# Optimization experiments

Measured on AMD Instinct MI355X. Metric: run time of the kernel, lower is better.

## Reference

```python
import jax, jax.numpy as jnp
import numpy as np
from jax import lax


def _conv(x, w, padding):
    # NCHW input, OIHW weights, stride 1, no bias
    return lax.conv_general_dilated(x, w, (1, 1), padding,
                                    dimension_numbers=('NCHW', 'OIHW', 'NCHW'))


def setup_inputs() -> dict:
    key = jax.random.key(0)
    ks = jax.random.split(key, 6)
    B, C, H, W = 16, 512, 40, 40
    return {
        'exemplar': jax.random.normal(ks[0], (B, C, H, W), jnp.float32),
        'query':    jax.random.normal(ks[1], (B, C, H, W), jnp.float32),
        'w_e':  jax.random.normal(ks[2], (256, C, 1, 1), jnp.float32) * 0.01,
        'w_q':  jax.random.normal(ks[3], (256, C, 1, 1), jnp.float32) * 0.01,
        'w_c1': jax.random.normal(ks[4], (C, C, 3, 3), jnp.float32) * 0.01,
        'w_c2': jax.random.normal(ks[5], (C, C, 3, 3), jnp.float32) * 0.01,
    }


def reference(exemplar, query, w_e, w_q, w_c1, w_c2):
    B, C, H, W = query.shape
    N = H * W
    # 1x1 projections to 256-dim correlation space
    q_corr = _conv(query, w_q, 'VALID').reshape(B, -1, N)     # [B,256,N]
    e_corr = _conv(exemplar, w_e, 'VALID').reshape(B, -1, N)  # [B,256,N]
    # A[b, n_exemplar, m_query] = <e_corr[:, n], q_corr[:, m]>
    A = jnp.einsum('bcn,bcm->bnm', e_corr, q_corr)            # [B,N,N]
    # A1 = softmax over exemplar axis, then transpose (torch: softmax(A,dim=1).T)
    A1 = jnp.swapaxes(jax.nn.softmax(A, axis=1), 1, 2)        # [B,N,N]
    # Bm = softmax(A^T, dim=1).T  == softmax(A, axis=2)
    Bm = jnp.swapaxes(jax.nn.softmax(jnp.swapaxes(A, 1, 2), axis=1), 1, 2)
    e_flat = exemplar.reshape(B, C, N)
    q_flat = query.reshape(B, C, N)
    query_att = jnp.matmul(e_flat, A1)   # [B,C,N]
    exemplar_att = jnp.matmul(q_flat, Bm)  # [B,C,N]
    input1_att = _conv(exemplar_att.reshape(B, C, H, W), w_c1, 'SAME')
    input2_att = _conv(query_att.reshape(B, C, H, W), w_c2, 'SAME')
    return jnp.concatenate([input1_att, input2_att], axis=1)  # [B,2C,H,W]
```

## Files before the change

### kernel.cpp

```cpp
#include <hip/hip_runtime.h>

typedef unsigned short u16;
typedef __attribute__((ext_vector_type(8))) short bf16x8;
typedef __attribute__((ext_vector_type(4))) float f32x4;

__device__ __forceinline__ u16 f2bf(float f) {
  union { float f; unsigned u; } v; v.f = f;
  unsigned u = v.u;
  u += 0x7fffu + ((u >> 16) & 1u);
  return (u16)(u >> 16);
}

__device__ __forceinline__ void gll16(const void* g, void* l) {
  __builtin_amdgcn_global_load_lds(
      (const __attribute__((address_space(1))) void*)g,
      (__attribute__((address_space(3))) void*)l, 16, 0, 0);
}

__global__ __launch_bounds__(256) void transp_cast_x2(const float* __restrict__ ex,
                                                      const float* __restrict__ qu,
                                                      u16* __restrict__ xte,
                                                      u16* __restrict__ xtq) {
  __shared__ float t[32][33];
  int z = blockIdx.z;
  int b = z & 15;
  const float* xb = (z < 16 ? ex : qu) + (size_t)b * 819200;
  u16* xtb = (z < 16 ? xte : xtq) + (size_t)b * 819200;
  int n0 = blockIdx.x * 32, c0 = blockIdx.y * 32;
  int tx = threadIdx.x & 31, ty = threadIdx.x >> 5;
#pragma unroll
  for (int k = 0; k < 4; k++) {
    int c = ty + k * 8;
    t[c][tx] = xb[(size_t)(c0 + c) * 1600 + n0 + tx];
  }
  __syncthreads();
#pragma unroll
  for (int k = 0; k < 4; k++) {
    int n = ty + k * 8;
    xtb[(size_t)(n0 + n) * 512 + c0 + tx] = f2bf(t[tx][n]);
  }
}

__global__ void cast_w(const float* __restrict__ we, const float* __restrict__ wq,
                       u16* __restrict__ oe, u16* __restrict__ oq) {
  int i = blockIdx.x * 256 + threadIdx.x;
  oe[i] = f2bf(we[i]);
  oq[i] = f2bf(wq[i]);
}

__global__ void repack_wc(const float* __restrict__ w1, const float* __restrict__ w2,
                          u16* __restrict__ o1, u16* __restrict__ o2) {
  const float* w = blockIdx.y ? w2 : w1;
  u16* wr = blockIdx.y ? o2 : o1;
  int idx = blockIdx.x * 256 + threadIdx.x;
  int o = idx / 4608;
  int r = idx - o * 4608;
  int t = r >> 9;
  int c = r & 511;
  wr[idx] = f2bf(w[o * 4608 + c * 9 + t]);
}

__global__ void zero_mem(uint4* __restrict__ p, long n) {
  long i = (long)blockIdx.x * blockDim.x + threadIdx.x;
  long stride = (long)gridDim.x * blockDim.x;
  uint4 z; z.x = 0; z.y = 0; z.z = 0; z.w = 0;
  for (; i < n; i += stride) p[i] = z;
}

template <int MODE>
__global__ __launch_bounds__(256) void gemm_bt64(
    const u16* __restrict__ A, const u16* __restrict__ B, u16* __restrict__ C,
    const u16* __restrict__ A2, const u16* __restrict__ B2, u16* __restrict__ C2,
    int M, int N, int K, long sA, long sB, long sC) {
  __shared__ u16 lds_a[128 * 64];
  __shared__ u16 lds_b[128 * 64];
  int tid = threadIdx.x;
  int z = blockIdx.z, b = z & 15;
  const u16* Ab = (z < 16 ? A : A2) + (size_t)b * sA;
  const u16* Bb = (z < 16 ? B : B2) + (size_t)b * sB;
  u16* Cb = (z < 16 ? C : C2) + (size_t)b * sC;
  int m0 = blockIdx.x * 128, n0 = blockIdx.y * 128;

  int rsub = tid >> 3;
  int gch = (tid & 7) ^ (rsub & 7);
  long Kb = (long)K * 2;
  const char* pa[4];
  const char* pb[4];
#pragma unroll
  for (int c = 0; c < 4; c++) {
    int ra = m0 + 32 * c + rsub; ra = ra < M ? ra : M - 1;
    int rb = n0 + 32 * c + rsub; rb = rb < N ? rb : N - 1;
    pa[c] = (const char*)Ab + (long)ra * Kb + gch * 16;
    pb[c] = (const char*)Bb + (long)rb * Kb + gch * 16;
  }

  const f32x4 fzero = {0.f, 0.f, 0.f, 0.f};
  f32x4 acc[4][4];
#pragma unroll
  for (int mi = 0; mi < 4; mi++)
#pragma unroll
    for (int ni = 0; ni < 4; ni++) acc[mi][ni] = fzero;

  int wid = tid >> 6, lane = tid & 63;
  int wm = wid & 1, wn = wid >> 1;
  int lrow = lane & 15, lquad = lane >> 4;
  int sl = lrow & 7;

  int ksteps = K >> 6;
  for (int ks = 0; ks < ksteps; ks++) {
#pragma unroll
    for (int c = 0; c < 4; c++) {
      gll16(pa[c], (char*)lds_a + c * 4096 + tid * 16);
      gll16(pb[c], (char*)lds_b + c * 4096 + tid * 16);
      pa[c] += 128; pb[c] += 128;
    }
    __syncthreads();
#pragma unroll
    for (int k2 = 0; k2 < 2; k2++) {
      int sel = ((k2 << 2) | lquad) ^ sl;
      bf16x8 bv[4];
#pragma unroll
      for (int ni = 0; ni < 4; ni++) {
        int rowb = wn * 64 + ni * 16 + lrow;
        bv[ni] = *(const bf16x8*)((const char*)lds_b + rowb * 128 + sel * 16);
      }
#pragma unroll
      for (int mi = 0; mi < 4; mi++) {
        int rowa = wm * 64 + mi * 16 + lrow;
        bf16x8 av = *(const bf16x8*)((const char*)lds_a + rowa * 128 + sel * 16);
#pragma unroll
        for (int ni = 0; ni < 4; ni++)
          acc[mi][ni] =
              __builtin_amdgcn_mfma_f32_16x16x32_bf16(av, bv[ni], acc[mi][ni], 0, 0, 0);
      }
    }
    __syncthreads();
  }

#pragma unroll
  for (int mi = 0; mi < 4; mi++) {
#pragma unroll
    for (int r = 0; r < 4; r++) {
      int i = m0 + wm * 64 + mi * 16 + lquad * 4 + r;
      if (i >= M) continue;
#pragma unroll
      for (int ni = 0; ni < 4; ni++) {
        int j = n0 + wn * 64 + ni * 16 + lrow;
        if (j >= N) continue;
        float v = acc[mi][ni][r];
        if (MODE == 2) {
          int y = i / 40, x = i - y * 40;
          Cb[(size_t)((y + 1) * 42 + (x + 1)) * 512 + j] = f2bf(v);
        } else {
          Cb[(size_t)i * N + j] = f2bf(v);
        }
      }
    }
  }
}

__global__ __launch_bounds__(256) void gemm_corr_exp(
    const u16* __restrict__ A, const u16* __restrict__ B, u16* __restrict__ E,
    u16* __restrict__ ET, float* __restrict__ Zrow, float* __restrict__ Zcol) {
  __shared__ u16 lds_a[128 * 64];
  __shared__ u16 lds_b[128 * 64];
  int tid = threadIdx.x;
  int b = blockIdx.z;
  const u16* Ab = A + (size_t)b * 409600;
  const u16* Bb = B + (size_t)b * 409600;
  u16* Eb = E + (size_t)b * 2560000;
  u16* ETb = ET + (size_t)b * 2560000;
  int m0 = blockIdx.x * 128, n0 = blockIdx.y * 128;

  int rsub = tid >> 3;
  int gch = (tid & 7) ^ (rsub & 7);
  const char* pa[4];
  const char* pb[4];
#pragma unroll
  for (int c = 0; c < 4; c++) {
    int ra = m0 + 32 * c + rsub; ra = ra < 1600 ? ra : 1599;
    int rb = n0 + 32 * c + rsub; rb = rb < 1600 ? rb : 1599;
    pa[c] = (const char*)(Ab + (size_t)ra * 256) + gch * 16;
    pb[c] = (const char*)(Bb + (size_t)rb * 256) + gch * 16;
  }

  const f32x4 fzero = {0.f, 0.f, 0.f, 0.f};
  f32x4 acc[4][4];
#pragma unroll
  for (int mi = 0; mi < 4; mi++)
#pragma unroll
    for (int ni = 0; ni < 4; ni++) acc[mi][ni] = fzero;

  int wid = tid >> 6, lane = tid & 63;
  int wm = wid & 1, wn = wid >> 1;
  int lrow = lane & 15, lquad = lane >> 4;
  int sl = lrow & 7;

  for (int ks = 0; ks < 4; ks++) {
#pragma unroll
    for (int c = 0; c < 4; c++) {
      gll16(pa[c], (char*)lds_a + c * 4096 + tid * 16);
      gll16(pb[c], (char*)lds_b + c * 4096 + tid * 16);
      pa[c] += 128; pb[c] += 128;
    }
    __syncthreads();
#pragma unroll
    for (int k2 = 0; k2 < 2; k2++) {
      int sel = ((k2 << 2) | lquad) ^ sl;
      bf16x8 bv[4];
#pragma unroll
      for (int ni = 0; ni < 4; ni++) {
        int rowb = wn * 64 + ni * 16 + lrow;
        bv[ni] = *(const bf16x8*)((const char*)lds_b + rowb * 128 + sel * 16);
      }
#pragma unroll
      for (int mi = 0; mi < 4; mi++) {
        int rowa = wm * 64 + mi * 16 + lrow;
        bf16x8 av = *(const bf16x8*)((const char*)lds_a + rowa * 128 + sel * 16);
#pragma unroll
        for (int ni = 0; ni < 4; ni++)
          acc[mi][ni] =
              __builtin_amdgcn_mfma_f32_16x16x32_bf16(av, bv[ni], acc[mi][ni], 0, 0, 0);
      }
    }
    __syncthreads();
  }

  const int TS = 136;
  u16* T = lds_a;
  float colacc[4] = {0.f, 0.f, 0.f, 0.f};
#pragma unroll
  for (int s = 0; s < 4; s++) {
    if (wm == (s >> 1)) {
      int smi0 = (s & 1) * 2;
#pragma unroll
      for (int mi2 = 0; mi2 < 2; mi2++) {
        int mi = smi0 + mi2;
        float rowp[4] = {0.f, 0.f, 0.f, 0.f};
#pragma unroll
        for (int ni = 0; ni < 4; ni++) {
          int j = n0 + wn * 64 + ni * 16 + lrow;
          bool jv = j < 1600;
#pragma unroll
          for (int r = 0; r < 4; r++) {
            int i = m0 + wm * 64 + mi * 16 + lquad * 4 + r;
            float e = __expf(acc[mi][ni][r]);
            T[(mi2 * 16 + lquad * 4 + r) * TS + wn * 64 + ni * 16 + lrow] = f2bf(e);
            rowp[r] += jv ? e : 0.f;
            colacc[ni] += (i < 1600) ? e : 0.f;
          }
        }
#pragma unroll
        for (int r = 0; r < 4; r++) {
          float v = rowp[r];
          v += __shfl_xor(v, 1);
          v += __shfl_xor(v, 2);
          v += __shfl_xor(v, 4);
          v += __shfl_xor(v, 8);
          int i = m0 + wm * 64 + mi * 16 + lquad * 4 + r;
          if (lrow == 0 && i < 1600) atomicAdd(&Zrow[b * 1600 + i], v);
        }
      }
    }
    __syncthreads();
#pragma unroll
    for (int p = 0; p < 2; p++) {
      int jj = tid + p * 256;
      int ml = jj >> 4, n8 = jj & 15;
      int gi = m0 + s * 32 + ml, gj = n0 + n8 * 8;
      if (gi < 1600 && gj < 1600)
        *(uint4*)(Eb + (size_t)gi * 1600 + gj) = *(const uint4*)&T[ml * TS + n8 * 8];
    }
#pragma unroll
    for (int p = 0; p < 4; p++) {
      int jj = tid + p * 256;
      int n = jj >> 3, m4 = jj & 7;
      int gm = m0 + s * 32 + m4 * 4, gn = n0 + n;
      if (gn < 1600 && gm < 1600) {
        ushort4 v;
        v.x = T[(m4 * 4 + 0) * TS + n];
        v.y = T[(m4 * 4 + 1) * TS + n];
        v.z = T[(m4 * 4 + 2) * TS + n];
        v.w = T[(m4 * 4 + 3) * TS + n];
        *(ushort4*)(ETb + (size_t)gn * 1600 + gm) = v;
      }
    }
    __syncthreads();
  }
#pragma unroll
  for (int ni = 0; ni < 4; ni++) {
    float v = colacc[ni];
    v += __shfl_xor(v, 16);
    v += __shfl_xor(v, 32);
    int j = n0 + wn * 64 + ni * 16 + lrow;
    if (lquad == 0 && j < 1600) atomicAdd(&Zcol[b * 1600 + j], v);
  }
}

__global__ void scale_div(const float* __restrict__ ex, const float* __restrict__ qu,
                          const float* __restrict__ Zcol, const float* __restrict__ Zrow,
                          u16* __restrict__ ebf, u16* __restrict__ qbf) {
  const float* x; const float* Z; u16* o;
  if (blockIdx.y == 0) { x = ex; Z = Zcol; o = ebf; }
  else { x = qu; Z = Zrow; o = qbf; }
  size_t idx = (size_t)blockIdx.x * 256 + threadIdx.x;
  int b = (int)(idx / 819200);
  int i = (int)(idx % 1600);
  o[idx] = f2bf(x[idx] / Z[b * 1600 + i]);
}

__global__ __launch_bounds__(256) void conv_gemm64(
    const u16* __restrict__ W1, const u16* __restrict__ ATT1,
    const u16* __restrict__ W2, const u16* __restrict__ ATT2,
    float* __restrict__ out) {
  __shared__ u16 lds_a[128 * 64];
  __shared__ u16 lds_b[128 * 64];
  int tid = threadIdx.x;
  int z = blockIdx.z, b = z & 15, sel2 = z >> 4;
  const u16* W = sel2 ? W2 : W1;
  const u16* attb = (sel2 ? ATT2 : ATT1) + (size_t)b * 903168;
  float* outb = out + (size_t)b * 1638400 + (size_t)(sel2 ? 512 : 0) * 1600;
  int p0 = blockIdx.x * 128, o0 = blockIdx.y * 128;

  int rsub = tid >> 3;
  int gch = (tid & 7) ^ (rsub & 7);
  const char* pa[4];
  const char* pb[4];
#pragma unroll
  for (int c = 0; c < 4; c++) {
    int ro = o0 + 32 * c + rsub;
    pa[c] = (const char*)(W + (size_t)ro * 4608) + gch * 16;
    int p = p0 + 32 * c + rsub; p = p < 1600 ? p : 1599;
    int y = p / 40, x = p - y * 40;
    pb[c] = (const char*)(attb + (size_t)(y * 42 + x) * 512) + gch * 16;
  }

  const f32x4 fzero = {0.f, 0.f, 0.f, 0.f};
  f32x4 acc[4][4];
#pragma unroll
  for (int mi = 0; mi < 4; mi++)
#pragma unroll
    for (int ni = 0; ni < 4; ni++) acc[mi][ni] = fzero;

  int wid = tid >> 6, lane = tid & 63;
  int wm = wid & 1, wn = wid >> 1;
  int lrow = lane & 15, lquad = lane >> 4;
  int sl = lrow & 7;

  int tapbyte = 0, dxc = 0;
  for (int t = 0; t < 9; t++) {
#pragma unroll 2
    for (int kc = 0; kc < 8; kc++) {
#pragma unroll
      for (int c = 0; c < 4; c++) {
        gll16(pa[c], (char*)lds_a + c * 4096 + tid * 16);
        gll16(pb[c] + tapbyte + kc * 128, (char*)lds_b + c * 4096 + tid * 16);
        pa[c] += 128;
      }
      __syncthreads();
#pragma unroll
      for (int k2 = 0; k2 < 2; k2++) {
        int sel = ((k2 << 2) | lquad) ^ sl;
        bf16x8 bv[4];
#pragma unroll
        for (int ni = 0; ni < 4; ni++) {
          int rowb = wn * 64 + ni * 16 + lrow;
          bv[ni] = *(const bf16x8*)((const char*)lds_b + rowb * 128 + sel * 16);
        }
#pragma unroll
        for (int mi = 0; mi < 4; mi++) {
          int rowa = wm * 64 + mi * 16 + lrow;
          bf16x8 av = *(const bf16x8*)((const char*)lds_a + rowa * 128 + sel * 16);
#pragma unroll
          for (int ni = 0; ni < 4; ni++)
            acc[mi][ni] = __builtin_amdgcn_mfma_f32_16x16x32_bf16(av, bv[ni],
                                                                  acc[mi][ni], 0, 0, 0);
        }
      }
      __syncthreads();
    }
    dxc++;
    tapbyte += 1024;
    if (dxc == 3) { dxc = 0; tapbyte += 39 * 1024; }
  }

#pragma unroll
  for (int mi = 0; mi < 4; mi++) {
#pragma unroll
    for (int r = 0; r < 4; r++) {
      int o = o0 + wm * 64 + mi * 16 + lquad * 4 + r;
#pragma unroll
      for (int ni = 0; ni < 4; ni++) {
        int p = p0 + wn * 64 + ni * 16 + lrow;
        if (p < 1600) outb[(size_t)o * 1600 + p] = acc[mi][ni][r];
      }
    }
  }
}

extern "C" void kernel_launch(void* const* d_in, const int* in_sizes, int n_in,
                              void* d_out, int out_size, void* d_ws, size_t ws_size,
                              hipStream_t stream) {
  const float* ex = (const float*)d_in[0];
  const float* qu = (const float*)d_in[1];
  const float* w_e = (const float*)d_in[2];
  const float* w_q = (const float*)d_in[3];
  const float* w_c1 = (const float*)d_in[4];
  const float* w_c2 = (const float*)d_in[5];
  float* out = (float*)d_out;
  char* ws = (char*)d_ws;

  u16* E     = (u16*)(ws + 0L);
  u16* ET    = (u16*)(ws + 81920000L);
  u16* xt_e  = (u16*)(ws + 163840000L);
  u16* xt_q  = (u16*)(ws + 190054400L);
  u16* ecorr = (u16*)(ws + 216268800L);
  u16* qcorr = (u16*)(ws + 229376000L);
  u16* att_e = (u16*)(ws + 242483200L);
  u16* att_q = (u16*)(ws + 271384576L);
  float* Zrow = (float*)(ws + 300285952L);
  float* Zcol = (float*)(ws + 300388352L);
  u16* w_ebf = (u16*)(ws + 300490752L);
  u16* w_qbf = (u16*)(ws + 300752896L);
  u16* wr1   = (u16*)(ws + 301015040L);
  u16* wr2   = (u16*)(ws + 305733632L);

  transp_cast_x2<<<dim3(50, 16, 32), 256, 0, stream>>>(ex, qu, xt_e, xt_q);
  cast_w<<<dim3(512), 256, 0, stream>>>(w_e, w_q, w_ebf, w_qbf);
  repack_wc<<<dim3(9216, 2), 256, 0, stream>>>(w_c1, w_c2, wr1, wr2);
  zero_mem<<<dim3(2048), 256, 0, stream>>>((uint4*)att_e, 3625472L);

  gemm_bt64<0><<<dim3(13, 2, 32), 256, 0, stream>>>(
      xt_e, w_ebf, ecorr, xt_q, w_qbf, qcorr, 1600, 256, 512, 819200L, 0L, 409600L);

  gemm_corr_exp<<<dim3(13, 13, 16), 256, 0, stream>>>(ecorr, qcorr, E, ET, Zrow, Zcol);

  u16* ebf = xt_e;
  u16* qbf = xt_q;
  scale_div<<<dim3(51200, 2), 256, 0, stream>>>(ex, qu, Zcol, Zrow, ebf, qbf);

  gemm_bt64<2><<<dim3(13, 4, 32), 256, 0, stream>>>(
      E, ebf, att_q, ET, qbf, att_e, 1600, 512, 1600, 2560000L, 819200L, 903168L);

  conv_gemm64<<<dim3(13, 4, 32), 256, 0, stream>>>(wr1, att_e, wr2, att_q, out);
}
```

Baseline: 930.5 us.

## Rewrite 3x3 conv GEMM with 256x256 tiles and 8-phase double-buffered pipeline

The implicit-GEMM 3x3 convolution kernel moves from 128x128 tiles with 256 threads to 256x256 tiles with 512 threads. Global-to-LDS loads are double-buffered and interleaved with MFMA phases using explicit waitcnt, barriers, sched_barrier and setprio. The goal is to raise arithmetic intensity per LDS byte and hide load latency behind compute. The larger tiles waste more work on the 1600-pixel edge (7x256 covers 1792), the grid shrinks to 448 blocks, and register pressure rises.

```diff
diff --git a/kernel.cpp b/kernel.cpp
--- a/kernel.cpp
+++ b/kernel.cpp
@@ -309,90 +309,140 @@
   o[idx] = f2bf(x[idx] / Z[b * 1600 + i]);
 }
 
-__global__ __launch_bounds__(256) void conv_gemm64(
+__global__ __launch_bounds__(512, 2) void conv_gemm8p(
     const u16* __restrict__ W1, const u16* __restrict__ ATT1,
     const u16* __restrict__ W2, const u16* __restrict__ ATT2,
     float* __restrict__ out) {
-  __shared__ u16 lds_a[128 * 64];
-  __shared__ u16 lds_b[128 * 64];
+  __shared__ u16 ldsA[32768];
+  __shared__ u16 ldsB[32768];
   int tid = threadIdx.x;
   int z = blockIdx.z, b = z & 15, sel2 = z >> 4;
   const u16* W = sel2 ? W2 : W1;
   const u16* attb = (sel2 ? ATT2 : ATT1) + (size_t)b * 903168;
   float* outb = out + (size_t)b * 1638400 + (size_t)(sel2 ? 512 : 0) * 1600;
-  int p0 = blockIdx.x * 128, o0 = blockIdx.y * 128;
-
-  int rsub = tid >> 3;
-  int gch = (tid & 7) ^ (rsub & 7);
-  const char* pa[4];
-  const char* pb[4];
-#pragma unroll
-  for (int c = 0; c < 4; c++) {
-    int ro = o0 + 32 * c + rsub;
-    pa[c] = (const char*)(W + (size_t)ro * 4608) + gch * 16;
-    int p = p0 + 32 * c + rsub; p = p < 1600 ? p : 1599;
-    int y = p / 40, x = p - y * 40;
-    pb[c] = (const char*)(attb + (size_t)(y * 42 + x) * 512) + gch * 16;
-  }
-
-  const f32x4 fzero = {0.f, 0.f, 0.f, 0.f};
-  f32x4 acc[4][4];
-#pragma unroll
-  for (int mi = 0; mi < 4; mi++)
-#pragma unroll
-    for (int ni = 0; ni < 4; ni++) acc[mi][ni] = fzero;
+  int p0 = blockIdx.x * 256, o0 = blockIdx.y * 256;
+
+  int rl = tid >> 2;
+  int cs = (tid & 3) ^ ((rl >> 1) & 3);
+  const char* pA0 = (const char*)(W + (size_t)(o0 + rl) * 4608) + cs * 16;
+  const char* pA1 = pA0 + 128 * 9216;
+  int pp0 = p0 + rl; pp0 = pp0 < 1600 ? pp0 : 1599;
+  int y0 = pp0 / 40, x0 = pp0 - y0 * 40;
+  const char* pB0 = (const char*)(attb + (size_t)(y0 * 42 + x0) * 512) + cs * 16;
+  int pp1 = p0 + 128 + rl; pp1 = pp1 < 1600 ? pp1 : 1599;
+  int y1 = pp1 / 40, x1 = pp1 - y1 * 40;
+  const char* pB1 = (const char*)(attb + (size_t)(y1 * 42 + x1) * 512) + cs * 16;
+
+  char* ldsAb = (char*)ldsA;
+  char* ldsBb = (char*)ldsB;
+  int dstT = tid * 16;
+
+#define STAGE_A(d, kh, kt)                                              \
+  {                                                                     \
+    int ko = (kt) * 128 + (kh) * 64;                                    \
+    gll16(pA0 + ko, ldsAb + ((d) * 2 + (kh)) * 16384 + dstT);           \
+    gll16(pA1 + ko, ldsAb + ((d) * 2 + (kh)) * 16384 + 8192 + dstT);    \
+  }
+#define STAGE_B(d, kh, kt)                                              \
+  {                                                                     \
+    int tp = (kt) >> 3;                                                 \
+    int ty = (tp * 11) >> 5;                                            \
+    int tx = tp - ty * 3;                                               \
+    int ko = (ty * 42 + tx) * 1024 + ((kt) & 7) * 128 + (kh) * 64;      \
+    gll16(pB0 + ko, ldsBb + ((d) * 2 + (kh)) * 16384 + dstT);           \
+    gll16(pB1 + ko, ldsBb + ((d) * 2 + (kh)) * 16384 + 8192 + dstT);    \
+  }
 
   int wid = tid >> 6, lane = tid & 63;
   int wm = wid & 1, wn = wid >> 1;
   int lrow = lane & 15, lquad = lane >> 4;
-  int sl = lrow & 7;
-
-  int tapbyte = 0, dxc = 0;
-  for (int t = 0; t < 9; t++) {
-#pragma unroll 2
-    for (int kc = 0; kc < 8; kc++) {
-#pragma unroll
-      for (int c = 0; c < 4; c++) {
-        gll16(pa[c], (char*)lds_a + c * 4096 + tid * 16);
-        gll16(pb[c] + tapbyte + kc * 128, (char*)lds_b + c * 4096 + tid * 16);
-        pa[c] += 128;
-      }
-      __syncthreads();
-#pragma unroll
-      for (int k2 = 0; k2 < 2; k2++) {
-        int sel = ((k2 << 2) | lquad) ^ sl;
-        bf16x8 bv[4];
-#pragma unroll
-        for (int ni = 0; ni < 4; ni++) {
-          int rowb = wn * 64 + ni * 16 + lrow;
-          bv[ni] = *(const bf16x8*)((const char*)lds_b + rowb * 128 + sel * 16);
-        }
-#pragma unroll
-        for (int mi = 0; mi < 4; mi++) {
-          int rowa = wm * 64 + mi * 16 + lrow;
-          bf16x8 av = *(const bf16x8*)((const char*)lds_a + rowa * 128 + sel * 16);
-#pragma unroll
-          for (int ni = 0; ni < 4; ni++)
-            acc[mi][ni] = __builtin_amdgcn_mfma_f32_16x16x32_bf16(av, bv[ni],
-                                                                  acc[mi][ni], 0, 0, 0);
-        }
-      }
-      __syncthreads();
-    }
-    dxc++;
-    tapbyte += 1024;
-    if (dxc == 3) { dxc = 0; tapbyte += 39 * 1024; }
-  }
-
-#pragma unroll
-  for (int mi = 0; mi < 4; mi++) {
+  int csel = (lquad ^ ((lrow >> 1) & 3)) << 4;
+  int aBase = (wm * 128 + lrow) * 64 + csel;
+  int bBase = (wn * 64 + lrow) * 64 + csel;
+
+  const f32x4 fzero = {0.f, 0.f, 0.f, 0.f};
+  f32x4 acc[8][4];
+#pragma unroll
+  for (int mi = 0; mi < 8; mi++)
+#pragma unroll
+    for (int ni = 0; ni < 4; ni++) acc[mi][ni] = fzero;
+
+  STAGE_B(0, 0, 0); STAGE_A(0, 0, 0); STAGE_B(0, 1, 0); STAGE_A(0, 1, 0);
+  STAGE_B(1, 0, 1); STAGE_A(1, 0, 1); STAGE_B(1, 1, 1);
+  asm volatile("s_waitcnt vmcnt(6)" ::: "memory");
+  __builtin_amdgcn_s_barrier();
+
+  bf16x8 bv0, bv1, bv2, bv3;
+
+#define MFMA4(mi, av)                                                          \
+  acc[mi][0] = __builtin_amdgcn_mfma_f32_16x16x32_bf16(av, bv0, acc[mi][0], 0, 0, 0); \
+  acc[mi][1] = __builtin_amdgcn_mfma_f32_16x16x32_bf16(av, bv1, acc[mi][1], 0, 0, 0); \
+  acc[mi][2] = __builtin_amdgcn_mfma_f32_16x16x32_bf16(av, bv2, acc[mi][2], 0, 0, 0); \
+  acc[mi][3] = __builtin_amdgcn_mfma_f32_16x16x32_bf16(av, bv3, acc[mi][3], 0, 0, 0);
+
+#define PHASE(d, kh, mh, STG, VM)                                              \
+  {                                                                            \
+    const char* ra_ = ldsAb + ((d) * 2 + (kh)) * 16384 + aBase + (mh) * 4096;  \
+    bf16x8 av0 = *(const bf16x8*)(ra_);                                        \
+    bf16x8 av1 = *(const bf16x8*)(ra_ + 1024);                                 \
+    bf16x8 av2 = *(const bf16x8*)(ra_ + 2048);                                 \
+    bf16x8 av3 = *(const bf16x8*)(ra_ + 3072);                                 \
+    if ((mh) == 0) {                                                           \
+      const char* rb_ = ldsBb + ((d) * 2 + (kh)) * 16384 + bBase;              \
+      bv0 = *(const bf16x8*)(rb_);                                             \
+      bv1 = *(const bf16x8*)(rb_ + 1024);                                      \
+      bv2 = *(const bf16x8*)(rb_ + 2048);                                      \
+      bv3 = *(const bf16x8*)(rb_ + 3072);                                      \
+    }                                                                          \
+    STG;                                                                       \
+    VM;                                                                        \
+    __builtin_amdgcn_s_barrier();                                              \
+    asm volatile("s_waitcnt lgkmcnt(0)" ::: "memory");                         \
+    __builtin_amdgcn_sched_barrier(0);                                         \
+    __builtin_amdgcn_s_setprio(1);                                             \
+    MFMA4((mh) * 4 + 0, av0);                                                  \
+    MFMA4((mh) * 4 + 1, av1);                                                  \
+    MFMA4((mh) * 4 + 2, av2);                                                  \
+    MFMA4((mh) * 4 + 3, av3);                                                  \
+    __builtin_amdgcn_s_setprio(0);                                             \
+    __builtin_amdgcn_sched_barrier(0);                                         \
+    __builtin_amdgcn_s_barrier();                                              \
+  }
+
+#define VMW asm volatile("s_waitcnt vmcnt(6)" ::: "memory")
+
+#pragma unroll 1
+  for (int it = 0; it < 36; ++it) {
+    int ktb = it * 2;
+    int kt1 = ktb + 1;
+    int kt2 = ktb + 2 < 72 ? ktb + 2 : 71;
+    int kt3 = ktb + 3 < 72 ? ktb + 3 : 71;
+    PHASE(0, 0, 0, STAGE_A(1, 1, kt1), (void)0);
+    PHASE(0, 0, 1, STAGE_B(0, 0, kt2), (void)0);
+    PHASE(0, 1, 0, STAGE_A(0, 0, kt2), (void)0);
+    PHASE(0, 1, 1, STAGE_B(0, 1, kt2), VMW);
+    PHASE(1, 0, 0, STAGE_A(0, 1, kt2), (void)0);
+    PHASE(1, 0, 1, STAGE_B(1, 0, kt3), (void)0);
+    PHASE(1, 1, 0, STAGE_A(1, 0, kt3), (void)0);
+    PHASE(1, 1, 1, STAGE_B(1, 1, kt3), VMW);
+  }
+
+#undef PHASE
+#undef MFMA4
+#undef VMW
+#undef STAGE_A
+#undef STAGE_B
+
+#pragma unroll
+  for (int mi = 0; mi < 8; mi++) {
 #pragma unroll
     for (int r = 0; r < 4; r++) {
-      int o = o0 + wm * 64 + mi * 16 + lquad * 4 + r;
+      int o = o0 + wm * 128 + mi * 16 + lquad * 4 + r;
+      float* orow = outb + (size_t)o * 1600;
 #pragma unroll
       for (int ni = 0; ni < 4; ni++) {
         int p = p0 + wn * 64 + ni * 16 + lrow;
-        if (p < 1600) outb[(size_t)o * 1600 + p] = acc[mi][ni][r];
+        if (p < 1600) orow[p] = acc[mi][ni][r];
       }
     }
   }
@@ -442,5 +492,5 @@
   gemm_bt64<2><<<dim3(13, 4, 32), 256, 0, stream>>>(
       E, ebf, att_q, ET, qbf, att_e, 1600, 512, 1600, 2560000L, 819200L, 903168L);
 
-  conv_gemm64<<<dim3(13, 4, 32), 256, 0, stream>>>(wr1, att_e, wr2, att_q, out);
-}
+  conv_gemm8p<<<dim3(7, 2, 32), 512, 0, stream>>>(wr1, att_e, wr2, att_q, out);
+}
```

Result: faster. 867.0 us (-6.8%).
